# Optimization experiments

Hardware: AMD Instinct MI355X
Metric: run time of the kernel (lower is better)

Reference implementation:

```python
import jax, jax.numpy as jnp
import numpy as np

B, O, L, N, V, H = 4, 4, 128, 8, 256, 256  # batch, options, max_len, topN, vec_size, hidden


def _gru(x, wih, whh, bih, bhh):
    """PyTorch-style GRU (gate order r,z,n), zero init hidden. x: [b,t,d] -> [b,t,H]."""
    xg = jnp.einsum('btd,gd->btg', x, wih) + bih  # input projections for all steps
    h0 = jnp.zeros((x.shape[0], whh.shape[1]), x.dtype)

    def step(h, xt):
        hg = h @ whh.T + bhh
        xr, xz, xn = jnp.split(xt, 3, axis=-1)
        hr, hz, hn = jnp.split(hg, 3, axis=-1)
        r = jax.nn.sigmoid(xr + hr)
        z = jax.nn.sigmoid(xz + hz)
        n = jnp.tanh(xn + r * hn)
        h = (1.0 - z) * n + z * h
        return h, h

    _, ys = jax.lax.scan(step, h0, jnp.swapaxes(xg, 0, 1))
    return jnp.swapaxes(ys, 0, 1)


def setup_inputs() -> dict:
    key = jax.random.key(0)
    ks = jax.random.split(key, 19)
    r = lambda k, s, sc=1.0: jax.random.normal(k, s, jnp.float32) * sc
    w = 0.05  # weight scale
    return {
        'statement': r(ks[0], (B, L, V)),
        'answer': r(ks[1], (B, O, L, V)),
        'refs': r(ks[2], (B, O, N, L, V)),
        'ctx_wih': r(ks[3], (3 * H, V), w), 'ctx_whh': r(ks[4], (3 * H, H), w),
        'ctx_bih': r(ks[5], (3 * H,), w), 'ctx_bhh': r(ks[6], (3 * H,), w),
        'sr_wih': r(ks[7], (3 * H, H), w), 'sr_whh': r(ks[8], (3 * H, H), w),
        'sr_bih': r(ks[9], (3 * H,), w), 'sr_bhh': r(ks[10], (3 * H,), w),
        'dr_wih': r(ks[11], (3 * H, 2 * H), w), 'dr_whh': r(ks[12], (3 * H, H), w),
        'dr_bih': r(ks[13], (3 * H,), w), 'dr_bhh': r(ks[14], (3 * H,), w),
        'gate_w': r(ks[15], (1, 2 * H), w), 'gate_b': r(ks[16], (1,), w),
        'out_w': r(ks[17], (1, 4 * H), w), 'out_b': r(ks[18], (1,), w),
    }


def reference(statement, answer, refs,
              ctx_wih, ctx_whh, ctx_bih, ctx_bhh,
              sr_wih, sr_whh, sr_bih, sr_bhh,
              dr_wih, dr_whh, dr_bih, dr_bhh,
              gate_w, gate_b, out_w, out_b):
    Ls = 2 * L
    # statement = cat(question, option) per option, context-encoded (option loop vectorized)
    q = jnp.broadcast_to(statement[:, None], (B, O, L, V))
    stmt = jnp.concatenate([q, answer], axis=2)  # [B,O,Ls,V]
    stmt = _gru(stmt.reshape(B * O, Ls, V), ctx_wih, ctx_whh, ctx_bih, ctx_bhh).reshape(B, O, Ls, H)
    docs = _gru(refs.reshape(B * O * N, L, V), ctx_wih, ctx_whh, ctx_bih, ctx_bhh).reshape(B, O, N, L, H)
    # statement-doc co-attention (doc loop vectorized)
    match = jnp.einsum('bosh,bonlh->bonsl', stmt, docs)  # [B,O,N,Ls,L]
    read_sum = jnp.einsum('bonsl,bonlh->bonsh', jax.nn.softmax(match, axis=-1), docs)  # [B,O,N,Ls,H]
    doc_read = jnp.einsum('bonsl,bosh->bonlh', jax.nn.softmax(match, axis=3), stmt)    # [B,O,N,L,H]
    dri = jnp.concatenate([docs, doc_read], axis=-1)  # [B,O,N,L,2H]
    # doc-doc cross attention against all topN*L positions
    flat = dri.reshape(B, O, N * L, 2 * H)
    mm = jnp.einsum('bonld,bomd->bonlm', dri, flat)  # [B,O,N,L,N*L]
    att = jnp.einsum('bonlm,bomd->bonld', jax.nn.softmax(mm, axis=-1), flat)  # [B,O,N,L,2H]
    # reasoning GRUs + max-pool over time
    s_r = _gru(read_sum.reshape(B * O * N, Ls, H), sr_wih, sr_whh, sr_bih, sr_bhh).max(axis=1).reshape(B, O, N, H)
    d_r = _gru(att.reshape(B * O * N, L, 2 * H), dr_wih, dr_whh, dr_bih, dr_bhh).max(axis=1).reshape(B, O, N, H)
    res = jnp.concatenate([s_r, d_r], axis=-1)  # [B,O,N,2H]
    coef = jnp.einsum('bond,ed->bone', res, gate_w) + gate_b  # [B,O,N,1] (no sigmoid, as in source)
    res = coef * res
    feat = jnp.concatenate([res.max(axis=2), res.mean(axis=2)], axis=-1)  # [B,O,4H]
    out = jnp.einsum('bod,ed->boe', feat, out_w)[..., 0] + out_b  # [B,O]
    return jax.nn.softmax(out, axis=1)
```

## Files before the change

### kernel.cpp

```cpp
#include <hip/hip_runtime.h>
#include <hip/hip_bf16.h>
#include <hip/hip_fp16.h>


typedef unsigned short u16;
typedef unsigned int u32;
typedef __attribute__((ext_vector_type(8))) short short8;
typedef __attribute__((ext_vector_type(4))) float floatx4;

__device__ __forceinline__ float bf2f(u16 v) { return __uint_as_float(((u32)v) << 16); }
__device__ __forceinline__ u16 f2b(float f) {
  u32 u = __float_as_uint(f);
  return (u16)((u + 0x7fffu + ((u >> 16) & 1u)) >> 16);
}
__device__ __forceinline__ float ldf(u16 v) { return bf2f(v); }
__device__ __forceinline__ float ldf(float v) { return v; }
__device__ __forceinline__ void stf(u16* p, float v) { *p = f2b(v); }
__device__ __forceinline__ void stf(float* p, float v) { *p = v; }
__device__ __forceinline__ float ldraw(const void* p, size_t i, int isf) {
  return isf ? ((const float*)p)[i] : bf2f(((const u16*)p)[i]);
}
__device__ __forceinline__ __half2 u2h(u32 v) {
  union { u32 u; __half2 h; } c; c.u = v; return c.h;
}

__global__ void k_detect(const void* __restrict__ stmt, int* __restrict__ flag) {
  if (threadIdx.x == 0 && blockIdx.x == 0) {
    const float* f = (const float*)stmt;
    int sane = 0;
    for (int i = 0; i < 64; ++i) {
      const float a = fabsf(f[i]);
      if (a > 1e-20f && a < 1e6f) sane++;
    }
    *flag = (sane >= 48) ? 1 : 0;
  }
}

__global__ __launch_bounds__(256) void k_cvt(const void* __restrict__ in, u16* __restrict__ out,
                                             int n, const int* __restrict__ flag) {
  const int isf = *flag;
  const int i = blockIdx.x * 256 + threadIdx.x;
  if (i < n) out[i] = f2b(ldraw(in, i, isf));
}

__global__ __launch_bounds__(256) void k_gather_stmt(const void* __restrict__ statement,
                                                     const void* __restrict__ answer,
                                                     u16* __restrict__ out,
                                                     const int* __restrict__ flag) {
  const int isf = *flag;
  const int idx = blockIdx.x * 256 + threadIdx.x;
  const int v = idx & 255;
  const int s = (idx >> 8) & 255;
  const int bo = idx >> 16;
  float val;
  if (s < 128) val = ldraw(statement, (size_t)(((bo >> 2) * 128) + s) * 256 + v, isf);
  else         val = ldraw(answer, (size_t)((bo * 128) + (s - 128)) * 256 + v, isf);
  out[idx] = f2b(val);
}

__global__ __launch_bounds__(256) void k_packh(const void* __restrict__ in, u32* __restrict__ out,
                                               int total, const int* __restrict__ flag) {
  const int isf = *flag;
  const int idx = blockIdx.x * 256 + threadIdx.x;
  if (idx >= total) return;
  const int r = idx % 768;
  const int k2 = idx / 768;
  const float a = ldraw(in, (size_t)r * 256 + 2 * k2, isf);
  const float b = ldraw(in, (size_t)r * 256 + 2 * k2 + 1, isf);
  const __half2 h2 = __floats2half2_rn(a, b);
  out[(((size_t)(k2 >> 2) * 768) + r) * 4 + (k2 & 3)] = *reinterpret_cast<const u32*>(&h2);
}

#define LOADW(i) uint4 w##i = wp[(i) * 768];
#define PINW(i) asm volatile("" : "+v"(w##i.x), "+v"(w##i.y), "+v"(w##i.z), "+v"(w##i.w));
#define STEPW(i)                                                             \
  {                                                                          \
    const uint4 hv = *reinterpret_cast<const uint4*>(&hs_h[(i) * 8]);        \
    a0 = __hfma2(u2h(w##i.x), u2h(hv.x), a0);                                \
    a1 = __hfma2(u2h(w##i.y), u2h(hv.y), a1);                                \
    a2 = __hfma2(u2h(w##i.z), u2h(hv.z), a2);                                \
    a3 = __hfma2(u2h(w##i.w), u2h(hv.w), a3);                                \
  }

__global__ __attribute__((amdgpu_flat_work_group_size(768, 768), amdgpu_waves_per_eu(3, 3)))
void k_rec(
    const u16* __restrict__ xg0, const u32* __restrict__ whh0,
    const u16* __restrict__ bih0, const u16* __restrict__ bhh0,
    u16* __restrict__ oseq0, float* __restrict__ omax0, int nseq0, int T0,
    const u16* __restrict__ xg1, const u32* __restrict__ whh1,
    const u16* __restrict__ bih1, const u16* __restrict__ bhh1,
    u16* __restrict__ oseq1, float* __restrict__ omax1, int T1) {
  const u16 *xg, *bih, *bhh; const u32* whh; u16* oseq; float* omax; int T, seq;
  if ((int)blockIdx.x < nseq0) {
    seq = blockIdx.x; xg = xg0; whh = whh0; bih = bih0; bhh = bhh0;
    oseq = oseq0; omax = omax0; T = T0;
  } else {
    seq = blockIdx.x - nseq0; xg = xg1; whh = whh1; bih = bih1; bhh = bhh1;
    oseq = oseq1; omax = omax1; T = T1;
  }
  __shared__ float hs_f[256];
  __shared__ __align__(16) __half hs_h[256];
  __shared__ float sh[768];
  const int t = threadIdx.x;
  const uint4* wp = reinterpret_cast<const uint4*>(whh) + t;
  LOADW(0)  LOADW(1)  LOADW(2)  LOADW(3)  LOADW(4)  LOADW(5)  LOADW(6)  LOADW(7)
  LOADW(8)  LOADW(9)  LOADW(10) LOADW(11) LOADW(12) LOADW(13) LOADW(14) LOADW(15)
  LOADW(16) LOADW(17) LOADW(18) LOADW(19) LOADW(20) LOADW(21) LOADW(22) LOADW(23)
  LOADW(24) LOADW(25) LOADW(26) LOADW(27) LOADW(28) LOADW(29) LOADW(30) LOADW(31)
  PINW(0)  PINW(1)  PINW(2)  PINW(3)  PINW(4)  PINW(5)  PINW(6)  PINW(7)
  PINW(8)  PINW(9)  PINW(10) PINW(11) PINW(12) PINW(13) PINW(14) PINW(15)
  PINW(16) PINW(17) PINW(18) PINW(19) PINW(20) PINW(21) PINW(22) PINW(23)
  PINW(24) PINW(25) PINW(26) PINW(27) PINW(28) PINW(29) PINW(30) PINW(31)
  const float bh = bf2f(bhh[t]);
  float bir = 0.f, biz = 0.f, bin = 0.f;
  if (t < 256) {
    bir = bf2f(bih[t]); biz = bf2f(bih[t + 256]); bin = bf2f(bih[t + 512]);
    hs_f[t] = 0.f;
    hs_h[t] = __float2half(0.f);
  }
  float vmax = -3.4e38f;
  const u16* xrow = xg + (size_t)seq * T * 768;
  for (int st = 0; st < T; ++st, xrow += 768) {
    float xr = 0.f, xz = 0.f, xn = 0.f;
    if (t < 256) {
      xr = bf2f(xrow[t]); xz = bf2f(xrow[t + 256]); xn = bf2f(xrow[t + 512]);
    }
    __syncthreads();
    __half2 a0 = __floats2half2_rn(0.f, 0.f), a1 = a0, a2 = a0, a3 = a0;
    STEPW(0)  STEPW(1)  STEPW(2)  STEPW(3)  STEPW(4)  STEPW(5)  STEPW(6)  STEPW(7)
    STEPW(8)  STEPW(9)  STEPW(10) STEPW(11) STEPW(12) STEPW(13) STEPW(14) STEPW(15)
    STEPW(16) STEPW(17) STEPW(18) STEPW(19) STEPW(20) STEPW(21) STEPW(22) STEPW(23)
    STEPW(24) STEPW(25) STEPW(26) STEPW(27) STEPW(28) STEPW(29) STEPW(30) STEPW(31)
    const float ah = (__low2float(a0) + __high2float(a0)) + (__low2float(a1) + __high2float(a1))
                   + (__low2float(a2) + __high2float(a2)) + (__low2float(a3) + __high2float(a3));
    sh[t] = ah + bh;
    __syncthreads();
    if (t < 256) {
      const float r = 1.f / (1.f + __expf(-(xr + bir + sh[t])));
      const float z = 1.f / (1.f + __expf(-(xz + biz + sh[t + 256])));
      const float n = tanhf(xn + bin + r * sh[t + 512]);
      const float hnew = (1.f - z) * n + z * hs_f[t];
      hs_f[t] = hnew;
      hs_h[t] = __float2half(hnew);
      if (oseq) oseq[(size_t)(seq * T + st) * 256 + t] = f2b(hnew);
      vmax = fmaxf(vmax, hnew);
    }
  }
  if (omax && t < 256) omax[(size_t)seq * 256 + t] = vmax;
}

template <bool BT, bool CADD, typename TA, typename TB, typename TC>
__global__ __launch_bounds__(256) void k_mgemm(
    const TA* __restrict__ Abase, int lda, long strideA, int divA,
    const TB* __restrict__ Bbase, int ldb, long strideB, int divB,
    TC* __restrict__ Cbase, int ldc, long strideC, int K) {
  const int z = blockIdx.z;
  const TA* A = Abase + (size_t)(z / divA) * strideA;
  const TB* Bp = Bbase + (size_t)(z / divB) * strideB;
  TC* C = Cbase + (size_t)z * strideC;
  const int m0 = blockIdx.y << 6, n0 = blockIdx.x << 6;
  __shared__ __align__(16) u16 As[2048];
  __shared__ __align__(16) u16 Bs[2048];
  const int t = threadIdx.x;
  const int lane = t & 63, w = t >> 6;
  floatx4 acc0 = {0.f, 0.f, 0.f, 0.f};
  floatx4 acc1 = {0.f, 0.f, 0.f, 0.f};
  floatx4 acc2 = {0.f, 0.f, 0.f, 0.f};
  floatx4 acc3 = {0.f, 0.f, 0.f, 0.f};
  const int ar = t >> 2;
  const int ac = (t & 3) << 3;
  const int adst = (((ar >> 4) << 6) | (ar & 15) | ((t & 3) << 4)) << 3;
  const int bk = t >> 3;
  const int bn = (t & 7) << 3;
  for (int k0 = 0; k0 < K; k0 += 32) {
    {
      const TA* ap = A + (size_t)(m0 + ar) * lda + (k0 + ac);
      if constexpr (sizeof(TA) == 2) {
        *reinterpret_cast<uint4*>(&As[adst]) = *reinterpret_cast<const uint4*>(ap);
      } else {
        const float4 f0 = reinterpret_cast<const float4*>(ap)[0];
        const float4 f1 = reinterpret_cast<const float4*>(ap)[1];
        u16* d = &As[adst];
        d[0] = f2b(f0.x); d[1] = f2b(f0.y); d[2] = f2b(f0.z); d[3] = f2b(f0.w);
        d[4] = f2b(f1.x); d[5] = f2b(f1.y); d[6] = f2b(f1.z); d[7] = f2b(f1.w);
      }
    }
    if constexpr (BT) {
      const TB* bp = Bp + (size_t)(n0 + ar) * ldb + (k0 + ac);
      *reinterpret_cast<uint4*>(&Bs[adst]) = *reinterpret_cast<const uint4*>(bp);
    } else {
      const TB* bp = Bp + (size_t)(k0 + bk) * ldb + (n0 + bn);
      const uint4 v = *reinterpret_cast<const uint4*>(bp);
      const u16* pv = reinterpret_cast<const u16*>(&v);
#pragma unroll
      for (int j = 0; j < 8; ++j) {
        const int n = bn + j;
        Bs[(((((n >> 4) << 6) | (n & 15) | ((bk >> 3) << 4)) << 3) | (bk & 7))] = pv[j];
      }
    }
    __syncthreads();
    const short8 af = *reinterpret_cast<const short8*>(&As[(w * 64 + lane) << 3]);
    const short8 b0 = *reinterpret_cast<const short8*>(&Bs[(lane) << 3]);
    const short8 b1 = *reinterpret_cast<const short8*>(&Bs[(64 + lane) << 3]);
    const short8 b2 = *reinterpret_cast<const short8*>(&Bs[(128 + lane) << 3]);
    const short8 b3 = *reinterpret_cast<const short8*>(&Bs[(192 + lane) << 3]);
    acc0 = __builtin_amdgcn_mfma_f32_16x16x32_bf16(af, b0, acc0, 0, 0, 0);
    acc1 = __builtin_amdgcn_mfma_f32_16x16x32_bf16(af, b1, acc1, 0, 0, 0);
    acc2 = __builtin_amdgcn_mfma_f32_16x16x32_bf16(af, b2, acc2, 0, 0, 0);
    acc3 = __builtin_amdgcn_mfma_f32_16x16x32_bf16(af, b3, acc3, 0, 0, 0);
    __syncthreads();
  }
  const int q = lane >> 4, cn = lane & 15;
  TC* crow = C + (size_t)(m0 + (w << 4) + (q << 2)) * ldc + n0 + cn;
#pragma unroll
  for (int i = 0; i < 4; ++i) {
    TC* cp = crow + (size_t)i * ldc;
    float v0 = acc0[i], v1 = acc1[i], v2 = acc2[i], v3 = acc3[i];
    if (CADD) { v0 += ldf(cp[0]); v1 += ldf(cp[16]); v2 += ldf(cp[32]); v3 += ldf(cp[48]); }
    stf(cp + 0, v0); stf(cp + 16, v1); stf(cp + 32, v2); stf(cp + 48, v3);
  }
}

template <typename TI, typename TO>
__global__ __launch_bounds__(256) void k_softmax_row(const TI* __restrict__ in,
                                                     TO* __restrict__ out, int Lrow) {
  const TI* p = in + (size_t)blockIdx.x * Lrow;
  TO* q = out + (size_t)blockIdx.x * Lrow;
  const int t = threadIdx.x;
  __shared__ float redA[4];
  __shared__ float redB[4];
  float m = -3.4e38f;
  for (int i = t; i < Lrow; i += 256) m = fmaxf(m, ldf(p[i]));
  for (int o = 32; o; o >>= 1) m = fmaxf(m, __shfl_xor(m, o, 64));
  if ((t & 63) == 0) redA[t >> 6] = m;
  __syncthreads();
  m = fmaxf(fmaxf(redA[0], redA[1]), fmaxf(redA[2], redA[3]));
  float s = 0.f;
  for (int i = t; i < Lrow; i += 256) {
    const float e = __expf(ldf(p[i]) - m);
    stf(q + i, e);
    s += e;
  }
  for (int o = 32; o; o >>= 1) s += __shfl_xor(s, o, 64);
  if ((t & 63) == 0) redB[t >> 6] = s;
  __syncthreads();
  s = redB[0] + redB[1] + redB[2] + redB[3];
  const float inv = 1.f / s;
  for (int i = t; i < Lrow; i += 256) stf(q + i, ldf(q[i]) * inv);
}

__global__ __launch_bounds__(256) void k_softmax_colT(const float* __restrict__ match,
                                                      u16* __restrict__ qT) {
  const int bon = blockIdx.x, l = blockIdx.y;
  const int t = threadIdx.x;
  __shared__ float redA[4];
  __shared__ float redB[4];
  const float x = match[((size_t)bon * 256 + t) * 128 + l];
  float m = x;
  for (int o = 32; o; o >>= 1) m = fmaxf(m, __shfl_xor(m, o, 64));
  if ((t & 63) == 0) redA[t >> 6] = m;
  __syncthreads();
  m = fmaxf(fmaxf(redA[0], redA[1]), fmaxf(redA[2], redA[3]));
  const float e = __expf(x - m);
  float s = e;
  for (int o = 32; o; o >>= 1) s += __shfl_xor(s, o, 64);
  if ((t & 63) == 0) redB[t >> 6] = s;
  __syncthreads();
  s = redB[0] + redB[1] + redB[2] + redB[3];
  qT[((size_t)bon * 128 + l) * 256 + t] = f2b(e / s);
}

__global__ __launch_bounds__(256) void k_final(
    const float* __restrict__ s_r, const float* __restrict__ d_r,
    const u16* __restrict__ gw, const u16* __restrict__ gb,
    const u16* __restrict__ ow, const u16* __restrict__ ob,
    void* __restrict__ out, const int* __restrict__ flag) {
  __shared__ float coef[128];
  __shared__ float logits[16];
  const int t = threadIdx.x;
  if (t < 128) {
    float acc = bf2f(gb[0]);
    const float* sp = s_r + (size_t)t * 256;
    const float* dp = d_r + (size_t)t * 256;
    for (int d = 0; d < 256; ++d) acc += bf2f(gw[d]) * sp[d];
    for (int d = 0; d < 256; ++d) acc += bf2f(gw[256 + d]) * dp[d];
    coef[t] = acc;
  }
  __syncthreads();
  if (t < 16) {
    float acc = bf2f(ob[0]);
    for (int d = 0; d < 512; ++d) {
      float mx = -3.4e38f, sm = 0.f;
      for (int n = 0; n < 8; ++n) {
        const int bon = t * 8 + n;
        const float base = (d < 256) ? s_r[(size_t)bon * 256 + d] : d_r[(size_t)bon * 256 + (d - 256)];
        const float v = coef[bon] * base;
        mx = fmaxf(mx, v);
        sm += v;
      }
      acc += bf2f(ow[d]) * mx + bf2f(ow[512 + d]) * (sm * 0.125f);
    }
    logits[t] = acc;
  }
  __syncthreads();
  if (t < 4) {
    const int isf = *flag;
    float m = -3.4e38f;
    for (int o = 0; o < 4; ++o) m = fmaxf(m, logits[t * 4 + o]);
    float e[4], s = 0.f;
    for (int o = 0; o < 4; ++o) { e[o] = __expf(logits[t * 4 + o] - m); s += e[o]; }
    for (int o = 0; o < 4; ++o) {
      const float v = e[o] / s;
      if (isf) ((float*)out)[t * 4 + o] = v;
      else     ((u16*)out)[t * 4 + o] = f2b(v);
    }
  }
}

extern "C" void kernel_launch(void* const* d_in, const int* in_sizes, int n_in,
                              void* d_out, int out_size, void* d_ws, size_t ws_size,
                              hipStream_t stream) {
  (void)in_sizes; (void)n_in; (void)out_size; (void)ws_size;
  const void* statement = d_in[0];
  const void* answer    = d_in[1];
  const void* refs      = d_in[2];
  const void* ctx_wih = d_in[3];
  const void* ctx_whh = d_in[4];
  const void* ctx_bih = d_in[5];
  const void* ctx_bhh = d_in[6];
  const void* sr_wih = d_in[7];
  const void* sr_whh = d_in[8];
  const void* sr_bih = d_in[9];
  const void* sr_bhh = d_in[10];
  const void* dr_wih = d_in[11];
  const void* dr_whh = d_in[12];
  const void* dr_bih = d_in[13];
  const void* dr_bhh = d_in[14];
  const void* gate_w = d_in[15];
  const void* gate_b = d_in[16];
  const void* out_w  = d_in[17];
  const void* out_b  = d_in[18];

  char* ws = (char*)d_ws;
  size_t off = 0;
  auto alloc = [&](size_t bytes) -> void* {
    void* p = ws + off;
    off += (bytes + 255) & ~(size_t)255;
    return p;
  };
  int* FLAG    = (int*)alloc(256);
  u16* CTXWIH  = (u16*)alloc((size_t)768 * 256 * 2);
  u16* SRWIH   = (u16*)alloc((size_t)768 * 256 * 2);
  u16* DRWIH   = (u16*)alloc((size_t)768 * 512 * 2);
  u32* CTXWHH2 = (u32*)alloc((size_t)128 * 768 * 4);
  u32* SRWHH2  = (u32*)alloc((size_t)128 * 768 * 4);
  u32* DRWHH2  = (u32*)alloc((size_t)128 * 768 * 4);
  u16* B_CTX_I = (u16*)alloc(768 * 2);
  u16* B_CTX_H = (u16*)alloc(768 * 2);
  u16* B_SR_I  = (u16*)alloc(768 * 2);
  u16* B_SR_H  = (u16*)alloc(768 * 2);
  u16* B_DR_I  = (u16*)alloc(768 * 2);
  u16* B_DR_H  = (u16*)alloc(768 * 2);
  u16* GW = (u16*)alloc(512 * 2);
  u16* GB = (u16*)alloc(2);
  u16* OW = (u16*)alloc(1024 * 2);
  u16* OB = (u16*)alloc(2);
  u16* STMT_H   = (u16*)alloc((size_t)16 * 256 * 256 * 2);
  u16* DOCS_H   = (u16*)alloc((size_t)128 * 128 * 256 * 2);
  u16* DOC_READ = (u16*)alloc((size_t)128 * 128 * 256 * 2);
  u16* ATT      = (u16*)alloc((size_t)128 * 128 * 512 * 2);
  float* SR_R = (float*)alloc((size_t)128 * 256 * 4);
  float* DR_R = (float*)alloc((size_t)128 * 256 * 4);
  const size_t ovl = off;
  u16* REFS_B   = (u16*)(ws + ovl);
  u16* STMT_IN  = (u16*)(ws + ovl + ((size_t)8 << 20));
  u16* XG_DOCS  = (u16*)(ws + ovl + ((size_t)16 << 20));
  u16* XG_STMT  = (u16*)(ws + ovl + ((size_t)41 << 20));
  float* MATCH  = (float*)(ws + ovl);
  u16* P_ROW    = (u16*)(ws + ovl + ((size_t)16 << 20));
  u16* MATCH_Q  = (u16*)(ws + ovl + ((size_t)24 << 20));
  u16* READ_SUM = (u16*)(ws + ovl + ((size_t)50 << 20));
  u16* XG_SR    = (u16*)(ws + ovl);
  float* MM     = (float*)(ws + ovl);
  u16* XG_DR    = (u16*)(ws + ovl);

  k_detect<<<1, 64, 0, stream>>>(statement, FLAG);

  k_gather_stmt<<<4096, 256, 0, stream>>>(statement, answer, STMT_IN, FLAG);
  k_cvt<<<16384, 256, 0, stream>>>(refs, REFS_B, 4194304, FLAG);
  k_cvt<<<768, 256, 0, stream>>>(ctx_wih, CTXWIH, 196608, FLAG);
  k_cvt<<<768, 256, 0, stream>>>(sr_wih, SRWIH, 196608, FLAG);
  k_cvt<<<1536, 256, 0, stream>>>(dr_wih, DRWIH, 393216, FLAG);
  k_packh<<<384, 256, 0, stream>>>(ctx_whh, CTXWHH2, 98304, FLAG);
  k_packh<<<384, 256, 0, stream>>>(sr_whh, SRWHH2, 98304, FLAG);
  k_packh<<<384, 256, 0, stream>>>(dr_whh, DRWHH2, 98304, FLAG);
  k_cvt<<<3, 256, 0, stream>>>(ctx_bih, B_CTX_I, 768, FLAG);
  k_cvt<<<3, 256, 0, stream>>>(ctx_bhh, B_CTX_H, 768, FLAG);
  k_cvt<<<3, 256, 0, stream>>>(sr_bih, B_SR_I, 768, FLAG);
  k_cvt<<<3, 256, 0, stream>>>(sr_bhh, B_SR_H, 768, FLAG);
  k_cvt<<<3, 256, 0, stream>>>(dr_bih, B_DR_I, 768, FLAG);
  k_cvt<<<3, 256, 0, stream>>>(dr_bhh, B_DR_H, 768, FLAG);
  k_cvt<<<2, 256, 0, stream>>>(gate_w, GW, 512, FLAG);
  k_cvt<<<1, 256, 0, stream>>>(gate_b, GB, 1, FLAG);
  k_cvt<<<4, 256, 0, stream>>>(out_w, OW, 1024, FLAG);
  k_cvt<<<1, 256, 0, stream>>>(out_b, OB, 1, FLAG);

  k_mgemm<true, false, u16, u16, u16><<<dim3(12, 64, 1), 256, 0, stream>>>(
      STMT_IN, 256, 0L, 1, CTXWIH, 256, 0L, 1, XG_STMT, 768, 0L, 256);
  k_mgemm<true, false, u16, u16, u16><<<dim3(12, 256, 1), 256, 0, stream>>>(
      REFS_B, 256, 0L, 1, CTXWIH, 256, 0L, 1, XG_DOCS, 768, 0L, 256);

  k_rec<<<144, 768, 0, stream>>>(
      XG_STMT, CTXWHH2, B_CTX_I, B_CTX_H, STMT_H, nullptr, 16, 256,
      XG_DOCS, CTXWHH2, B_CTX_I, B_CTX_H, DOCS_H, nullptr, 128);

  k_mgemm<true, false, u16, u16, float><<<dim3(2, 4, 128), 256, 0, stream>>>(
      STMT_H, 256, 65536L, 8, DOCS_H, 256, 32768L, 1, MATCH, 128, 32768L, 256);

  k_softmax_colT<<<dim3(128, 128), 256, 0, stream>>>(MATCH, MATCH_Q);
  k_softmax_row<float, u16><<<32768, 256, 0, stream>>>(MATCH, P_ROW, 128);

  k_mgemm<false, false, u16, u16, u16><<<dim3(4, 4, 128), 256, 0, stream>>>(
      P_ROW, 128, 32768L, 1, DOCS_H, 256, 32768L, 1, READ_SUM, 256, 65536L, 128);

  k_mgemm<false, false, u16, u16, u16><<<dim3(4, 2, 128), 256, 0, stream>>>(
      MATCH_Q, 256, 32768L, 1, STMT_H, 256, 65536L, 8, DOC_READ, 256, 32768L, 256);

  k_mgemm<true, false, u16, u16, u16><<<dim3(12, 512, 1), 256, 0, stream>>>(
      READ_SUM, 256, 0L, 1, SRWIH, 256, 0L, 1, XG_SR, 768, 0L, 256);

  k_rec<<<128, 768, 0, stream>>>(
      XG_SR, SRWHH2, B_SR_I, B_SR_H, nullptr, SR_R, 128, 256,
      nullptr, nullptr, nullptr, nullptr, nullptr, nullptr, 0);

  k_mgemm<true, false, u16, u16, float><<<dim3(16, 16, 16), 256, 0, stream>>>(
      DOCS_H, 256, 262144L, 1, DOCS_H, 256, 262144L, 1, MM, 1024, 1048576L, 256);
  k_mgemm<true, true, u16, u16, float><<<dim3(16, 16, 16), 256, 0, stream>>>(
      DOC_READ, 256, 262144L, 1, DOC_READ, 256, 262144L, 1, MM, 1024, 1048576L, 256);

  k_softmax_row<float, float><<<16384, 256, 0, stream>>>(MM, MM, 1024);

  k_mgemm<false, false, float, u16, u16><<<dim3(4, 16, 16), 256, 0, stream>>>(
      MM, 1024, 1048576L, 1, DOCS_H, 256, 262144L, 1, ATT, 512, 524288L, 1024);
  k_mgemm<false, false, float, u16, u16><<<dim3(4, 16, 16), 256, 0, stream>>>(
      MM, 1024, 1048576L, 1, DOC_READ, 256, 262144L, 1, ATT + 256, 512, 524288L, 1024);

  k_mgemm<true, false, u16, u16, u16><<<dim3(12, 256, 1), 256, 0, stream>>>(
      ATT, 512, 0L, 1, DRWIH, 512, 0L, 1, XG_DR, 768, 0L, 512);

  k_rec<<<128, 768, 0, stream>>>(
      XG_DR, DRWHH2, B_DR_I, B_DR_H, nullptr, DR_R, 128, 128,
      nullptr, nullptr, nullptr, nullptr, nullptr, nullptr, 0);

  k_final<<<1, 256, 0, stream>>>(SR_R, DR_R, GW, GB, OW, OB, d_out, FLAG);
}
```

Measured before the change: 1.732 ms.

## Store GRU recurrent weights as FP8 and stream them from memory each step

The recurrent weight matrix is repacked into FP8 (four values per 32-bit word) instead of FP16 pairs. The recurrence kernel no longer pins the whole weight slice in registers. Each timestep it reloads the packed weights through the cache, expands them to fp32 with packed conversion instructions, and accumulates against an fp32 hidden state read from shared memory. The aim is to cut register pressure and weight bytes while moving the dot-product arithmetic to fp32. In exchange it adds a global/cache load and conversions on every step, and FP8 weights lose accuracy.

```diff
diff --git a/kernel.cpp b/kernel.cpp
--- a/kernel.cpp
+++ b/kernel.cpp
@@ -7,6 +7,7 @@
 typedef unsigned int u32;
 typedef __attribute__((ext_vector_type(8))) short short8;
 typedef __attribute__((ext_vector_type(4))) float floatx4;
+typedef __attribute__((ext_vector_type(2))) float floatx2;
 
 __device__ __forceinline__ float bf2f(u16 v) { return __uint_as_float(((u32)v) << 16); }
 __device__ __forceinline__ u16 f2b(float f) {
@@ -19,9 +20,6 @@
 __device__ __forceinline__ void stf(float* p, float v) { *p = v; }
 __device__ __forceinline__ float ldraw(const void* p, size_t i, int isf) {
   return isf ? ((const float*)p)[i] : bf2f(((const u16*)p)[i]);
-}
-__device__ __forceinline__ __half2 u2h(u32 v) {
-  union { u32 u; __half2 h; } c; c.u = v; return c.h;
 }
 
 __global__ void k_detect(const void* __restrict__ stmt, int* __restrict__ flag) {
@@ -58,38 +56,30 @@
   out[idx] = f2b(val);
 }
 
-__global__ __launch_bounds__(256) void k_packh(const void* __restrict__ in, u32* __restrict__ out,
-                                               int total, const int* __restrict__ flag) {
+__global__ __launch_bounds__(256) void k_packf8(const void* __restrict__ in, u32* __restrict__ out,
+                                                const int* __restrict__ flag) {
   const int isf = *flag;
   const int idx = blockIdx.x * 256 + threadIdx.x;
-  if (idx >= total) return;
   const int r = idx % 768;
-  const int k2 = idx / 768;
-  const float a = ldraw(in, (size_t)r * 256 + 2 * k2, isf);
-  const float b = ldraw(in, (size_t)r * 256 + 2 * k2 + 1, isf);
-  const __half2 h2 = __floats2half2_rn(a, b);
-  out[(((size_t)(k2 >> 2) * 768) + r) * 4 + (k2 & 3)] = *reinterpret_cast<const u32*>(&h2);
-}
-
-#define LOADW(i) uint4 w##i = wp[(i) * 768];
-#define PINW(i) asm volatile("" : "+v"(w##i.x), "+v"(w##i.y), "+v"(w##i.z), "+v"(w##i.w));
-#define STEPW(i)                                                             \
-  {                                                                          \
-    const uint4 hv = *reinterpret_cast<const uint4*>(&hs_h[(i) * 8]);        \
-    a0 = __hfma2(u2h(w##i.x), u2h(hv.x), a0);                                \
-    a1 = __hfma2(u2h(w##i.y), u2h(hv.y), a1);                                \
-    a2 = __hfma2(u2h(w##i.z), u2h(hv.z), a2);                                \
-    a3 = __hfma2(u2h(w##i.w), u2h(hv.w), a3);                                \
-  }
-
-__global__ __attribute__((amdgpu_flat_work_group_size(768, 768), amdgpu_waves_per_eu(3, 3)))
-void k_rec(
+  const int k4 = idx / 768;
+  const float v0 = ldraw(in, (size_t)r * 256 + 4 * k4 + 0, isf);
+  const float v1 = ldraw(in, (size_t)r * 256 + 4 * k4 + 1, isf);
+  const float v2 = ldraw(in, (size_t)r * 256 + 4 * k4 + 2, isf);
+  const float v3 = ldraw(in, (size_t)r * 256 + 4 * k4 + 3, isf);
+  int pk = __builtin_amdgcn_cvt_pk_fp8_f32(v0, v1, 0, false);
+  pk = __builtin_amdgcn_cvt_pk_fp8_f32(v2, v3, pk, true);
+  out[(size_t)k4 * 768 + r] = (u32)pk;
+}
+
+__global__ __launch_bounds__(768, 3) void k_rec(
     const u16* __restrict__ xg0, const u32* __restrict__ whh0,
     const u16* __restrict__ bih0, const u16* __restrict__ bhh0,
     u16* __restrict__ oseq0, float* __restrict__ omax0, int nseq0, int T0,
     const u16* __restrict__ xg1, const u32* __restrict__ whh1,
     const u16* __restrict__ bih1, const u16* __restrict__ bhh1,
     u16* __restrict__ oseq1, float* __restrict__ omax1, int T1) {
+  __shared__ __align__(16) float hs_f[256];
+  __shared__ float sh[768];
   const u16 *xg, *bih, *bhh; const u32* whh; u16* oseq; float* omax; int T, seq;
   if ((int)blockIdx.x < nseq0) {
     seq = blockIdx.x; xg = xg0; whh = whh0; bih = bih0; bhh = bhh0;
@@ -98,42 +88,37 @@
     seq = blockIdx.x - nseq0; xg = xg1; whh = whh1; bih = bih1; bhh = bhh1;
     oseq = oseq1; omax = omax1; T = T1;
   }
-  __shared__ float hs_f[256];
-  __shared__ __align__(16) __half hs_h[256];
-  __shared__ float sh[768];
   const int t = threadIdx.x;
-  const uint4* wp = reinterpret_cast<const uint4*>(whh) + t;
-  LOADW(0)  LOADW(1)  LOADW(2)  LOADW(3)  LOADW(4)  LOADW(5)  LOADW(6)  LOADW(7)
-  LOADW(8)  LOADW(9)  LOADW(10) LOADW(11) LOADW(12) LOADW(13) LOADW(14) LOADW(15)
-  LOADW(16) LOADW(17) LOADW(18) LOADW(19) LOADW(20) LOADW(21) LOADW(22) LOADW(23)
-  LOADW(24) LOADW(25) LOADW(26) LOADW(27) LOADW(28) LOADW(29) LOADW(30) LOADW(31)
-  PINW(0)  PINW(1)  PINW(2)  PINW(3)  PINW(4)  PINW(5)  PINW(6)  PINW(7)
-  PINW(8)  PINW(9)  PINW(10) PINW(11) PINW(12) PINW(13) PINW(14) PINW(15)
-  PINW(16) PINW(17) PINW(18) PINW(19) PINW(20) PINW(21) PINW(22) PINW(23)
-  PINW(24) PINW(25) PINW(26) PINW(27) PINW(28) PINW(29) PINW(30) PINW(31)
   const float bh = bf2f(bhh[t]);
   float bir = 0.f, biz = 0.f, bin = 0.f;
   if (t < 256) {
     bir = bf2f(bih[t]); biz = bf2f(bih[t + 256]); bin = bf2f(bih[t + 512]);
     hs_f[t] = 0.f;
-    hs_h[t] = __float2half(0.f);
   }
   float vmax = -3.4e38f;
   const u16* xrow = xg + (size_t)seq * T * 768;
+  const u32* wbase = whh + t;
   for (int st = 0; st < T; ++st, xrow += 768) {
     float xr = 0.f, xz = 0.f, xn = 0.f;
     if (t < 256) {
       xr = bf2f(xrow[t]); xz = bf2f(xrow[t + 256]); xn = bf2f(xrow[t + 512]);
     }
     __syncthreads();
-    __half2 a0 = __floats2half2_rn(0.f, 0.f), a1 = a0, a2 = a0, a3 = a0;
-    STEPW(0)  STEPW(1)  STEPW(2)  STEPW(3)  STEPW(4)  STEPW(5)  STEPW(6)  STEPW(7)
-    STEPW(8)  STEPW(9)  STEPW(10) STEPW(11) STEPW(12) STEPW(13) STEPW(14) STEPW(15)
-    STEPW(16) STEPW(17) STEPW(18) STEPW(19) STEPW(20) STEPW(21) STEPW(22) STEPW(23)
-    STEPW(24) STEPW(25) STEPW(26) STEPW(27) STEPW(28) STEPW(29) STEPW(30) STEPW(31)
-    const float ah = (__low2float(a0) + __high2float(a0)) + (__low2float(a1) + __high2float(a1))
-                   + (__low2float(a2) + __high2float(a2)) + (__low2float(a3) + __high2float(a3));
-    sh[t] = ah + bh;
+    const u32* wsp = wbase;
+    asm volatile("" : "+v"(wsp));
+    floatx2 a01 = {0.f, 0.f}, a23 = {0.f, 0.f};
+#pragma unroll
+    for (int c = 0; c < 64; ++c) {
+      const u32 w = wsp[(size_t)c * 768];
+      const floatx2 f01 = __builtin_amdgcn_cvt_pk_f32_fp8(w, false);
+      const floatx2 f23 = __builtin_amdgcn_cvt_pk_f32_fp8(w, true);
+      const float4 h4 = *reinterpret_cast<const float4*>(&hs_f[c << 2]);
+      floatx2 h01; h01.x = h4.x; h01.y = h4.y;
+      floatx2 h23; h23.x = h4.z; h23.y = h4.w;
+      a01 += f01 * h01;
+      a23 += f23 * h23;
+    }
+    sh[t] = (a01.x + a01.y) + (a23.x + a23.y) + bh;
     __syncthreads();
     if (t < 256) {
       const float r = 1.f / (1.f + __expf(-(xr + bir + sh[t])));
@@ -141,7 +126,6 @@
       const float n = tanhf(xn + bin + r * sh[t + 512]);
       const float hnew = (1.f - z) * n + z * hs_f[t];
       hs_f[t] = hnew;
-      hs_h[t] = __float2half(hnew);
       if (oseq) oseq[(size_t)(seq * T + st) * 256 + t] = f2b(hnew);
       vmax = fmaxf(vmax, hnew);
     }
@@ -352,9 +336,9 @@
   u16* CTXWIH  = (u16*)alloc((size_t)768 * 256 * 2);
   u16* SRWIH   = (u16*)alloc((size_t)768 * 256 * 2);
   u16* DRWIH   = (u16*)alloc((size_t)768 * 512 * 2);
-  u32* CTXWHH2 = (u32*)alloc((size_t)128 * 768 * 4);
-  u32* SRWHH2  = (u32*)alloc((size_t)128 * 768 * 4);
-  u32* DRWHH2  = (u32*)alloc((size_t)128 * 768 * 4);
+  u32* CTXWHH8 = (u32*)alloc((size_t)64 * 768 * 4);
+  u32* SRWHH8  = (u32*)alloc((size_t)64 * 768 * 4);
+  u32* DRWHH8  = (u32*)alloc((size_t)64 * 768 * 4);
   u16* B_CTX_I = (u16*)alloc(768 * 2);
   u16* B_CTX_H = (u16*)alloc(768 * 2);
   u16* B_SR_I  = (u16*)alloc(768 * 2);
@@ -391,9 +375,9 @@
   k_cvt<<<768, 256, 0, stream>>>(ctx_wih, CTXWIH, 196608, FLAG);
   k_cvt<<<768, 256, 0, stream>>>(sr_wih, SRWIH, 196608, FLAG);
   k_cvt<<<1536, 256, 0, stream>>>(dr_wih, DRWIH, 393216, FLAG);
-  k_packh<<<384, 256, 0, stream>>>(ctx_whh, CTXWHH2, 98304, FLAG);
-  k_packh<<<384, 256, 0, stream>>>(sr_whh, SRWHH2, 98304, FLAG);
-  k_packh<<<384, 256, 0, stream>>>(dr_whh, DRWHH2, 98304, FLAG);
+  k_packf8<<<192, 256, 0, stream>>>(ctx_whh, CTXWHH8, FLAG);
+  k_packf8<<<192, 256, 0, stream>>>(sr_whh, SRWHH8, FLAG);
+  k_packf8<<<192, 256, 0, stream>>>(dr_whh, DRWHH8, FLAG);
   k_cvt<<<3, 256, 0, stream>>>(ctx_bih, B_CTX_I, 768, FLAG);
   k_cvt<<<3, 256, 0, stream>>>(ctx_bhh, B_CTX_H, 768, FLAG);
   k_cvt<<<3, 256, 0, stream>>>(sr_bih, B_SR_I, 768, FLAG);
@@ -411,8 +395,8 @@
       REFS_B, 256, 0L, 1, CTXWIH, 256, 0L, 1, XG_DOCS, 768, 0L, 256);
 
   k_rec<<<144, 768, 0, stream>>>(
-      XG_STMT, CTXWHH2, B_CTX_I, B_CTX_H, STMT_H, nullptr, 16, 256,
-      XG_DOCS, CTXWHH2, B_CTX_I, B_CTX_H, DOCS_H, nullptr, 128);
+      XG_STMT, CTXWHH8, B_CTX_I, B_CTX_H, STMT_H, nullptr, 16, 256,
+      XG_DOCS, CTXWHH8, B_CTX_I, B_CTX_H, DOCS_H, nullptr, 128);
 
   k_mgemm<true, false, u16, u16, float><<<dim3(2, 4, 128), 256, 0, stream>>>(
       STMT_H, 256, 65536L, 8, DOCS_H, 256, 32768L, 1, MATCH, 128, 32768L, 256);
@@ -430,7 +414,7 @@
       READ_SUM, 256, 0L, 1, SRWIH, 256, 0L, 1, XG_SR, 768, 0L, 256);
 
   k_rec<<<128, 768, 0, stream>>>(
-      XG_SR, SRWHH2, B_SR_I, B_SR_H, nullptr, SR_R, 128, 256,
+      XG_SR, SRWHH8, B_SR_I, B_SR_H, nullptr, SR_R, 128, 256,
       nullptr, nullptr, nullptr, nullptr, nullptr, nullptr, 0);
 
   k_mgemm<true, false, u16, u16, float><<<dim3(16, 16, 16), 256, 0, stream>>>(
@@ -449,7 +433,7 @@
       ATT, 512, 0L, 1, DRWIH, 512, 0L, 1, XG_DR, 768, 0L, 512);
 
   k_rec<<<128, 768, 0, stream>>>(
-      XG_DR, DRWHH2, B_DR_I, B_DR_H, nullptr, DR_R, 128, 128,
+      XG_DR, DRWHH8, B_DR_I, B_DR_H, nullptr, DR_R, 128, 128,
       nullptr, nullptr, nullptr, nullptr, nullptr, nullptr, 0);
 
   k_final<<<1, 256, 0, stream>>>(SR_R, DR_R, GW, GB, OW, OB, d_out, FLAG);
```

Result: slower. 2.964 ms (+71.1%).
